# Performance work log

Hardware: AMD Instinct MI355X
Metric: run time of the kernel (lower is better)

The kernel has to match this reference:

```python
import jax, jax.numpy as jnp
import numpy as np

D = 1024
H = 16
HD = D // H


def setup_inputs() -> dict:
    key = jax.random.key(0)
    ks = jax.random.split(key, 5)
    s = 1.0 / np.sqrt(D)
    return {
        "inputs": jax.random.normal(ks[0], (2, 2048, D), dtype=jnp.float32),
        "Wq": jax.random.normal(ks[1], (D, D), dtype=jnp.float32) * s,
        "bq": jnp.zeros((D,), jnp.float32),
        "Wk": jax.random.normal(ks[2], (D, D), dtype=jnp.float32) * s,
        "bk": jnp.zeros((D,), jnp.float32),
        "Wv": jax.random.normal(ks[3], (D, D), dtype=jnp.float32) * s,
        "bv": jnp.zeros((D,), jnp.float32),
        "Wo": jax.random.normal(ks[4], (D, D), dtype=jnp.float32) * s,
        "bo": jnp.zeros((D,), jnp.float32),
    }


def reference(inputs, Wq, bq, Wk, bk, Wv, bv, Wo, bo):
    B, S, _ = inputs.shape
    def split_heads(x):  # [B,S,D] -> [B,H,S,hd]
        return x.reshape(B, S, H, HD).transpose(0, 2, 1, 3)
    q = split_heads(inputs @ Wq + bq)
    k = split_heads(inputs @ Wk + bk)
    v = split_heads(inputs @ Wv + bv)
    scale = 1.0 / jnp.sqrt(jnp.asarray(HD, inputs.dtype))
    scores = jnp.einsum("bhsd,bhtd->bhst", q, k) * scale  # [B,H,S,S]
    weights = jax.nn.softmax(scores, axis=-1)
    attn = jnp.einsum("bhst,bhtd->bhsd", weights, v)
    concat = attn.transpose(0, 2, 1, 3).reshape(B, S, D)
    return concat @ Wo + bo
```

## Files before the change

kernel.cpp:

```cpp
#include <hip/hip_runtime.h>


typedef __bf16 bf16x8 __attribute__((ext_vector_type(8)));
typedef float  f32x4  __attribute__((ext_vector_type(4)));

#if __has_builtin(__builtin_amdgcn_exp2f)
#define EXPFN(x) __builtin_amdgcn_exp2f(x)
#define QSCALE (0.125f * 1.44269504088896f)
#else
#define EXPFN(x) __expf(x)
#define QSCALE 0.125f
#endif

#define VMCNT(n)  asm volatile("s_waitcnt vmcnt(" #n ")" ::: "memory")
#define LGKMCNT0() asm volatile("s_waitcnt lgkmcnt(0)" ::: "memory")
#define BARRIER() __builtin_amdgcn_s_barrier()
#define WAIT0_BARRIER() asm volatile("s_waitcnt vmcnt(0)\n\ts_barrier" ::: "memory")

__device__ __forceinline__ unsigned short f2bf(float f) {
    unsigned int u = __float_as_uint(f);
    u += 0x7FFFu + ((u >> 16) & 1u);
    return (unsigned short)(u >> 16);
}

__device__ __forceinline__ void gload16(const void* g, void* l) {
    __builtin_amdgcn_global_load_lds(
        (const __attribute__((address_space(1))) void*)g,
        (__attribute__((address_space(3))) void*)l, 16, 0, 0);
}

__global__ __launch_bounds__(256) void prep_kernel(
    const float* __restrict__ X, ushort4* __restrict__ Xb,
    const float* __restrict__ Wq, const float* __restrict__ Wk,
    const float* __restrict__ Wv, const float* __restrict__ Wo,
    unsigned short* __restrict__ Wt_all) {
    const int z = blockIdx.z;
    if (z == 4) {
        int base = (blockIdx.y * 32 + blockIdx.x) * 1024 + threadIdx.x;
        const float4* X4 = (const float4*)X;
        #pragma unroll
        for (int c = 0; c < 4; c++) {
            int i = base + c * 256;
            float4 v = X4[i];
            ushort4 o;
            o.x = f2bf(v.x); o.y = f2bf(v.y); o.z = f2bf(v.z); o.w = f2bf(v.w);
            Xb[i] = o;
        }
        return;
    }
    __shared__ float tile[32][33];
    const float* W = (z == 0) ? Wq : (z == 1) ? Wk : (z == 2) ? Wv : Wo;
    unsigned short* Wt = Wt_all + (size_t)z * 1024 * 1024;
    int c0 = blockIdx.x * 32, r0 = blockIdx.y * 32;
    int x = threadIdx.x & 31, y = threadIdx.x >> 5;
    for (int j = 0; j < 32; j += 8)
        tile[y + j][x] = W[(r0 + y + j) * 1024 + c0 + x];
    __syncthreads();
    for (int j = 0; j < 32; j += 8)
        Wt[(c0 + y + j) * 1024 + r0 + x] = f2bf(tile[x][y + j]);
}

__global__ __launch_bounds__(256, 2) void gemm_qkv_kernel(
    const unsigned short* __restrict__ Xb, const unsigned short* __restrict__ Wt_all,
    const float* __restrict__ bq, const float* __restrict__ bk,
    const float* __restrict__ bv,
    unsigned short* __restrict__ Qb, unsigned short* __restrict__ Kb,
    unsigned short* __restrict__ Vt) {
    const int x0 = blockIdx.x * 128;
    const int y0 = blockIdx.y * 64;

    __shared__ __align__(16) unsigned short smem[128 * 64 + 3 * 64 * 64];
    unsigned short* As  = smem;
    unsigned short* Bqs = smem + 8192;
    unsigned short* Bks = smem + 12288;
    unsigned short* Bvs = smem + 16384;

    const unsigned short* Ap  = Xb + (size_t)x0 * 1024;
    const unsigned short* Bqp = Wt_all + (size_t)y0 * 1024;
    const unsigned short* Bkp = Wt_all + 1048576u + (size_t)y0 * 1024;
    const unsigned short* Bvp = Wt_all + 2097152u + (size_t)y0 * 1024;

    const int tid = threadIdx.x;
    const int lane = tid & 63, wave = tid >> 6;
    const int quad = lane >> 4, l15 = lane & 15;
    const int wrow = (wave >> 1) * 64, wcol = (wave & 1) * 32;

    f32x4 aq[4][2] = {};
    f32x4 ak[4][2] = {};
    f32x4 av[4][2] = {};

    const int srow = lane >> 3;
    const int ch8  = (lane & 7) * 8;
    const int swz  = (((lane & 7) ^ srow)) * 8;
    const int sw   = (l15 & 7);

    for (int k0 = 0; k0 < 1024; k0 += 64) {
        #pragma unroll
        for (int c = 0; c < 4; c++) {
            int r = c * 32 + wave * 8 + srow;
            gload16(Ap + (size_t)r * 1024 + k0 + swz, &As[r * 64 + ch8]);
        }
        #pragma unroll
        for (int c = 0; c < 2; c++) {
            int r = c * 32 + wave * 8 + srow;
            gload16(Bqp + (size_t)r * 1024 + k0 + swz, &Bqs[r * 64 + ch8]);
            gload16(Bkp + (size_t)r * 1024 + k0 + swz, &Bks[r * 64 + ch8]);
            gload16(Bvp + (size_t)r * 1024 + k0 + swz, &Bvs[r * 64 + ch8]);
        }
        WAIT0_BARRIER();
        #pragma unroll
        for (int kk = 0; kk < 2; kk++) {
            bf16x8 af[4], bqf[2], bkf[2], bvf[2];
            const int co = (((kk * 4 + quad) ^ sw)) * 8;
            #pragma unroll
            for (int i = 0; i < 4; i++)
                af[i] = *(const bf16x8*)&As[(wrow + i * 16 + l15) * 64 + co];
            #pragma unroll
            for (int j = 0; j < 2; j++) {
                bqf[j] = *(const bf16x8*)&Bqs[(wcol + j * 16 + l15) * 64 + co];
                bkf[j] = *(const bf16x8*)&Bks[(wcol + j * 16 + l15) * 64 + co];
                bvf[j] = *(const bf16x8*)&Bvs[(wcol + j * 16 + l15) * 64 + co];
            }
            #pragma unroll
            for (int i = 0; i < 4; i++)
                #pragma unroll
                for (int j = 0; j < 2; j++) {
                    aq[i][j] = __builtin_amdgcn_mfma_f32_16x16x32_bf16(
                        af[i], bqf[j], aq[i][j], 0, 0, 0);
                    ak[i][j] = __builtin_amdgcn_mfma_f32_16x16x32_bf16(
                        af[i], bkf[j], ak[i][j], 0, 0, 0);
                    av[i][j] = __builtin_amdgcn_mfma_f32_16x16x32_bf16(
                        af[i], bvf[j], av[i][j], 0, 0, 0);
                }
        }
        __syncthreads();
    }

    #pragma unroll
    for (int j = 0; j < 2; j++) {
        int col = y0 + wcol + j * 16 + l15;
        float bqc = bq[col], bkc = bk[col];
        int h = col >> 6, d = col & 63;
        #pragma unroll
        for (int i = 0; i < 4; i++)
            #pragma unroll
            for (int r = 0; r < 4; r++) {
                int row = x0 + wrow + i * 16 + quad * 4 + r;
                int b = row >> 11, s = row & 2047;
                size_t idx = (size_t)((b * 16 + h) * 2048 + s) * 64 + d;
                Qb[idx] = f2bf((aq[i][j][r] + bqc) * QSCALE);
                Kb[idx] = f2bf(ak[i][j][r] + bkc);
            }
    }

    __syncthreads();
    unsigned short* vts = smem;
    #pragma unroll
    for (int j = 0; j < 2; j++) {
        int n = wcol + j * 16 + l15;
        float bvc = bv[y0 + n];
        #pragma unroll
        for (int i = 0; i < 4; i++)
            #pragma unroll
            for (int r = 0; r < 4; r++) {
                int m = wrow + i * 16 + quad * 4 + r;
                vts[n * 136 + m] = f2bf(av[i][j][r] + bvc);
            }
    }
    __syncthreads();
    const int bseq = x0 >> 11;
    const int s0 = x0 & 2047;
    #pragma unroll
    for (int q = 0; q < 4; q++) {
        int c = q * 256 + tid;
        int n = c >> 4, mc = c & 15;
        uint4 vv = *(const uint4*)&vts[n * 136 + mc * 8];
        *(uint4*)&Vt[(size_t)(bseq * 1024 + y0 + n) * 2048 + s0 + mc * 8] = vv;
    }
}

__global__ __launch_bounds__(256) void attn_kernel(
    const unsigned short* __restrict__ Qb, const unsigned short* __restrict__ Kb,
    const unsigned short* __restrict__ Vt, unsigned short* __restrict__ Cc,
    float* __restrict__ Op, float* __restrict__ Lp, int tlen, int do_split) {
    const int bh = blockIdx.y;
    const int b = bh >> 4, h = bh & 15;
    const int q0 = blockIdx.x * 128;
    const int split = blockIdx.z;
    const int tbeg = split * tlen;

    const int tid = threadIdx.x;
    const int lane = tid & 63, wave = tid >> 6;
    const int quad = lane >> 4, l15 = lane & 15;

    __shared__ __align__(16) unsigned short Ks[2][64 * 64];
    __shared__ __align__(16) unsigned short Vs[2][64 * 64];

    const unsigned short* Qbh = Qb + (size_t)bh * 2048 * 64;
    const unsigned short* Kbh = Kb + (size_t)bh * 2048 * 64;
    const unsigned short* Vbh = Vt + (size_t)bh * 64 * 2048;

    bf16x8 qa[2][2];
    #pragma unroll
    for (int mi = 0; mi < 2; mi++)
        #pragma unroll
        for (int kk = 0; kk < 2; kk++)
            qa[mi][kk] = *(const bf16x8*)&Qbh[
                (size_t)(q0 + wave * 32 + mi * 16 + l15) * 64 + kk * 32 + quad * 8];

    union { unsigned short us[8]; bf16x8 v; } ones_u;
    #pragma unroll
    for (int i = 0; i < 8; i++) ones_u.us[i] = 0x3F80;
    const bf16x8 onesv = ones_u.v;

    f32x4 o[2][4] = {};
    f32x4 ol[2] = {};

    const int srow = lane >> 3;
    const int r0s = wave * 16 + srow;
    const int ch8 = (lane & 7) * 8;
    const int swz = (((lane & 7) ^ srow)) * 8;
    const int sw  = (l15 & 7);

    const int pk0 = (r0s & 0x23) | ((r0s & 0x0C) << 1) | ((r0s & 0x10) >> 2);
    const int r8  = r0s + 8;
    const int pk8 = (r8 & 0x23) | ((r8 & 0x0C) << 1) | ((r8 & 0x10) >> 2);

    auto stage = [&](int buf, int t0) {
        gload16(&Kbh[(size_t)(t0 + pk0) * 64 + swz],       &Ks[buf][r0s * 64 + ch8]);
        gload16(&Kbh[(size_t)(t0 + pk8) * 64 + swz],       &Ks[buf][(r0s + 8) * 64 + ch8]);
        gload16(&Vbh[(size_t)r0s * 2048 + t0 + swz],       &Vs[buf][r0s * 64 + ch8]);
        gload16(&Vbh[(size_t)(r0s + 8) * 2048 + t0 + swz], &Vs[buf][(r0s + 8) * 64 + ch8]);
    };

    stage(0, tbeg);
    int cur = 0;
    for (int ti = 0; ti < tlen; ti += 64) {
        if (ti + 64 < tlen) {
            stage(cur ^ 1, tbeg + ti + 64);
            VMCNT(4);
        } else {
            VMCNT(0);
        }
        BARRIER();
        const unsigned short* Ksc = Ks[cur];
        const unsigned short* Vsc = Vs[cur];

        f32x4 sf[2][4] = {};
        #pragma unroll
        for (int j = 0; j < 4; j++)
            #pragma unroll
            for (int kk = 0; kk < 2; kk++) {
                bf16x8 kf = *(const bf16x8*)&Ksc[(j * 16 + l15) * 64 +
                                                 (((kk * 4 + quad) ^ sw)) * 8];
                sf[0][j] = __builtin_amdgcn_mfma_f32_16x16x32_bf16(kf, qa[0][kk], sf[0][j], 0, 0, 0);
                sf[1][j] = __builtin_amdgcn_mfma_f32_16x16x32_bf16(kf, qa[1][kk], sf[1][j], 0, 0, 0);
            }

        union { unsigned int u[4]; bf16x8 v; } pa[2][2];
        #pragma unroll
        for (int mi = 0; mi < 2; mi++) {
            float pe[4][4];
            #pragma unroll
            for (int j = 0; j < 4; j++)
                #pragma unroll
                for (int r = 0; r < 4; r++)
                    pe[j][r] = EXPFN(sf[mi][j][r]);
            #pragma unroll
            for (int kk = 0; kk < 2; kk++)
                #pragma unroll
                for (int d = 0; d < 4; d++) {
                    const int j = 2 * kk + (d >> 1);
                    const int r = 2 * (d & 1);
                    unsigned int w;
                    asm("v_cvt_pk_bf16_f32 %0, %1, %2"
                        : "=v"(w) : "v"(pe[j][r]), "v"(pe[j][r + 1]));
                    pa[mi][kk].u[d] = w;
                }
        }

        #pragma unroll
        for (int kk = 0; kk < 2; kk++) {
            bf16x8 pf0 = pa[0][kk].v;
            bf16x8 pf1 = pa[1][kk].v;
            ol[0] = __builtin_amdgcn_mfma_f32_16x16x32_bf16(pf0, onesv, ol[0], 0, 0, 0);
            ol[1] = __builtin_amdgcn_mfma_f32_16x16x32_bf16(pf1, onesv, ol[1], 0, 0, 0);
            #pragma unroll
            for (int j = 0; j < 4; j++) {
                bf16x8 vf = *(const bf16x8*)&Vsc[(j * 16 + l15) * 64 +
                                                 (((kk * 4 + quad) ^ sw)) * 8];
                o[0][j] = __builtin_amdgcn_mfma_f32_16x16x32_bf16(pf0, vf, o[0][j], 0, 0, 0);
                o[1][j] = __builtin_amdgcn_mfma_f32_16x16x32_bf16(pf1, vf, o[1][j], 0, 0, 0);
            }
        }
        LGKMCNT0();
        BARRIER();
        cur ^= 1;
    }

    if (do_split) {
        float* Opd = Op + (size_t)(split * 32 + bh) * 2048 * 64;
        float* Lpd = Lp + (size_t)(split * 32 + bh) * 2048;
        #pragma unroll
        for (int mi = 0; mi < 2; mi++)
            #pragma unroll
            for (int r = 0; r < 4; r++) {
                int s = q0 + wave * 32 + mi * 16 + quad * 4 + r;
                if (l15 == 0) Lpd[s] = ol[mi][r];
                #pragma unroll
                for (int j = 0; j < 4; j++)
                    Opd[(size_t)s * 64 + j * 16 + l15] = o[mi][j][r];
            }
    } else {
        #pragma unroll
        for (int mi = 0; mi < 2; mi++)
            #pragma unroll
            for (int r = 0; r < 4; r++) {
                float inv = 1.f / ol[mi][r];
                int s = q0 + wave * 32 + mi * 16 + quad * 4 + r;
                size_t row = (size_t)(b * 2048 + s);
                #pragma unroll
                for (int j = 0; j < 4; j++)
                    Cc[row * 1024 + h * 64 + j * 16 + l15] = f2bf(o[mi][j][r] * inv);
            }
    }
}

__global__ __launch_bounds__(256) void combine_kernel(
    const float4* __restrict__ Op, const float* __restrict__ Lp,
    unsigned short* __restrict__ Cc) {
    int idx = blockIdx.x * 256 + threadIdx.x;
    int d4 = idx & 15;
    int s = (idx >> 4) & 2047;
    int bh = idx >> 15;
    const size_t half4 = (size_t)32 * 2048 * 16;
    float4 a = Op[(size_t)idx], c = Op[half4 + (size_t)idx];
    float l = Lp[bh * 2048 + s] + Lp[32 * 2048 + bh * 2048 + s];
    float inv = 1.f / l;
    ushort4 o;
    o.x = f2bf((a.x + c.x) * inv); o.y = f2bf((a.y + c.y) * inv);
    o.z = f2bf((a.z + c.z) * inv); o.w = f2bf((a.w + c.w) * inv);
    int b = bh >> 4, h = bh & 15;
    *(ushort4*)&Cc[((size_t)(b * 2048 + s)) * 1024 + h * 64 + d4 * 4] = o;
}

__global__ __launch_bounds__(256) void gemm_out_kernel(
    const unsigned short* __restrict__ Cc, const unsigned short* __restrict__ Wot,
    const float* __restrict__ bo, float* __restrict__ out) {
    const int m0 = blockIdx.x * 128;
    const int n0 = blockIdx.y * 64;

    __shared__ __align__(16) unsigned short As[128 * 64];
    __shared__ __align__(16) unsigned short Bs[64 * 64];

    const int tid = threadIdx.x;
    const int lane = tid & 63, wave = tid >> 6;
    const int quad = lane >> 4, l15 = lane & 15;
    const int wrow = (wave >> 1) * 64, wcol = (wave & 1) * 32;

    f32x4 acc[4][2] = {};
    const int srow = lane >> 3;
    const int ch8 = (lane & 7) * 8;
    const int swz = (((lane & 7) ^ srow)) * 8;
    const int sw  = (l15 & 7);

    for (int k0 = 0; k0 < 1024; k0 += 64) {
        #pragma unroll
        for (int c = 0; c < 4; c++) {
            int r = c * 32 + wave * 8 + srow;
            gload16(Cc + (size_t)(m0 + r) * 1024 + k0 + swz, &As[r * 64 + ch8]);
            if (c < 2)
                gload16(Wot + (size_t)(n0 + r) * 1024 + k0 + swz, &Bs[r * 64 + ch8]);
        }
        WAIT0_BARRIER();
        #pragma unroll
        for (int kk = 0; kk < 2; kk++) {
            bf16x8 af[4], bfr[2];
            #pragma unroll
            for (int i = 0; i < 4; i++)
                af[i] = *(const bf16x8*)&As[(wrow + i * 16 + l15) * 64 +
                                            (((kk * 4 + quad) ^ sw)) * 8];
            #pragma unroll
            for (int j = 0; j < 2; j++)
                bfr[j] = *(const bf16x8*)&Bs[(wcol + j * 16 + l15) * 64 +
                                             (((kk * 4 + quad) ^ sw)) * 8];
            #pragma unroll
            for (int i = 0; i < 4; i++)
                #pragma unroll
                for (int j = 0; j < 2; j++)
                    acc[i][j] = __builtin_amdgcn_mfma_f32_16x16x32_bf16(
                        af[i], bfr[j], acc[i][j], 0, 0, 0);
        }
        __syncthreads();
    }

    #pragma unroll
    for (int j = 0; j < 2; j++) {
        int col = n0 + wcol + j * 16 + l15;
        float bcol = bo[col];
        #pragma unroll
        for (int i = 0; i < 4; i++)
            #pragma unroll
            for (int r = 0; r < 4; r++) {
                int row = m0 + wrow + i * 16 + quad * 4 + r;
                out[(size_t)row * 1024 + col] = acc[i][j][r] + bcol;
            }
    }
}

extern "C" void kernel_launch(void* const* d_in, const int* in_sizes, int n_in,
                              void* d_out, int out_size, void* d_ws, size_t ws_size,
                              hipStream_t stream) {
    const float* X  = (const float*)d_in[0];
    const float* Wq = (const float*)d_in[1];
    const float* bq = (const float*)d_in[2];
    const float* Wk = (const float*)d_in[3];
    const float* bk = (const float*)d_in[4];
    const float* Wv = (const float*)d_in[5];
    const float* bv = (const float*)d_in[6];
    const float* Wo = (const float*)d_in[7];
    const float* bo = (const float*)d_in[8];
    float* out = (float*)d_out;

    char* ws = (char*)d_ws;
    unsigned short* Xb = (unsigned short*)(ws);
    unsigned short* Wt = (unsigned short*)(ws + (8u  << 20));
    unsigned short* Qb = (unsigned short*)(ws + (16u << 20));
    unsigned short* Kb = (unsigned short*)(ws + (24u << 20));
    unsigned short* Vt = (unsigned short*)(ws + (32u << 20));
    unsigned short* Cc = (unsigned short*)(ws + (40u << 20));
    float* Op = (float*)(ws + (48u << 20));
    float* Lp = (float*)(ws + (48u << 20) + 33554432u);
    const bool use_split = ws_size >= ((size_t)(48u << 20) + 33554432u + 524288u);

    prep_kernel<<<dim3(32, 32, 5), 256, 0, stream>>>(X, (ushort4*)Xb, Wq, Wk, Wv, Wo, Wt);
    gemm_qkv_kernel<<<dim3(32, 16), 256, 0, stream>>>(Xb, Wt, bq, bk, bv, Qb, Kb, Vt);
    if (use_split) {
        attn_kernel<<<dim3(16, 32, 2), 256, 0, stream>>>(Qb, Kb, Vt, Cc, Op, Lp, 1024, 1);
        combine_kernel<<<4096, 256, 0, stream>>>((const float4*)Op, Lp, Cc);
    } else {
        attn_kernel<<<dim3(16, 32, 1), 256, 0, stream>>>(Qb, Kb, Vt, Cc, Op, Lp, 2048, 0);
    }
    gemm_out_kernel<<<dim3(32, 16), 256, 0, stream>>>(Cc, Wt + 3u * 1024 * 1024, bo, out);
}
```

Baseline: 186.1 us.

## Remap block indices for XCD-aware L2 locality and add MFMA priority hints

Block IDs in the QKV GEMM, attention and output GEMM kernels are remapped so that blocks dispatched round-robin to the same XCD share weight columns or the same (batch, head) K/V data. The aim is better reuse in each XCD's private L2. The attention kernel also raises wave priority around its MFMA sections with s_setprio, so matrix work is favoured over the softmax exponent phase of other waves. The remap hardcodes the grid shapes (32x16 GEMM grids, 16x32xZ attention grid) and would silently break if the launch dimensions change.

Measured after the change: 191.5 us. 1.03x slower.

```diff
diff --git a/kernel.cpp b/kernel.cpp
--- a/kernel.cpp
+++ b/kernel.cpp
@@ -66,8 +66,12 @@
     const float* __restrict__ bv,
     unsigned short* __restrict__ Qb, unsigned short* __restrict__ Kb,
     unsigned short* __restrict__ Vt) {
-    const int x0 = blockIdx.x * 128;
-    const int y0 = blockIdx.y * 64;
+    const int n = blockIdx.x + 32 * blockIdx.y;
+    const int xcd = n & 7, s = n >> 3;
+    const int yb = xcd * 2 + (s >> 5);
+    const int xb = s & 31;
+    const int x0 = xb * 128;
+    const int y0 = yb * 64;
 
     __shared__ __align__(16) unsigned short smem[128 * 64 + 3 * 64 * 64];
     unsigned short* As  = smem;
@@ -146,8 +150,8 @@
             #pragma unroll
             for (int r = 0; r < 4; r++) {
                 int row = x0 + wrow + i * 16 + quad * 4 + r;
-                int b = row >> 11, s = row & 2047;
-                size_t idx = (size_t)((b * 16 + h) * 2048 + s) * 64 + d;
+                int b = row >> 11, s2 = row & 2047;
+                size_t idx = (size_t)((b * 16 + h) * 2048 + s2) * 64 + d;
                 Qb[idx] = f2bf((aq[i][j][r] + bqc) * QSCALE);
                 Kb[idx] = f2bf(ak[i][j][r] + bkc);
             }
@@ -157,14 +161,14 @@
     unsigned short* vts = smem;
     #pragma unroll
     for (int j = 0; j < 2; j++) {
-        int n = wcol + j * 16 + l15;
-        float bvc = bv[y0 + n];
+        int nn = wcol + j * 16 + l15;
+        float bvc = bv[y0 + nn];
         #pragma unroll
         for (int i = 0; i < 4; i++)
             #pragma unroll
             for (int r = 0; r < 4; r++) {
                 int m = wrow + i * 16 + quad * 4 + r;
-                vts[n * 136 + m] = f2bf(av[i][j][r] + bvc);
+                vts[nn * 136 + m] = f2bf(av[i][j][r] + bvc);
             }
     }
     __syncthreads();
@@ -173,9 +177,9 @@
     #pragma unroll
     for (int q = 0; q < 4; q++) {
         int c = q * 256 + tid;
-        int n = c >> 4, mc = c & 15;
-        uint4 vv = *(const uint4*)&vts[n * 136 + mc * 8];
-        *(uint4*)&Vt[(size_t)(bseq * 1024 + y0 + n) * 2048 + s0 + mc * 8] = vv;
+        int nn = c >> 4, mc = c & 15;
+        uint4 vv = *(const uint4*)&vts[nn * 136 + mc * 8];
+        *(uint4*)&Vt[(size_t)(bseq * 1024 + y0 + nn) * 2048 + s0 + mc * 8] = vv;
     }
 }
 
@@ -183,10 +187,16 @@
     const unsigned short* __restrict__ Qb, const unsigned short* __restrict__ Kb,
     const unsigned short* __restrict__ Vt, unsigned short* __restrict__ Cc,
     float* __restrict__ Op, float* __restrict__ Lp, int tlen, int do_split) {
-    const int bh = blockIdx.y;
+    const int zs = do_split ? 2 : 1;
+    const int n = blockIdx.x + 16 * (blockIdx.y + 32 * blockIdx.z);
+    const int xcd = n & 7, sl = n >> 3;
+    const int G = zs * 4;
+    const int g = xcd * G + (sl >> 4);
+    const int bh = g & 31;
+    const int split = g >> 5;
+    const int q0 = (sl & 15) * 128;
+
     const int b = bh >> 4, h = bh & 15;
-    const int q0 = blockIdx.x * 128;
-    const int split = blockIdx.z;
     const int tbeg = split * tlen;
 
     const int tid = threadIdx.x;
@@ -247,6 +257,7 @@
         const unsigned short* Vsc = Vs[cur];
 
         f32x4 sf[2][4] = {};
+        __builtin_amdgcn_s_setprio(1);
         #pragma unroll
         for (int j = 0; j < 4; j++)
             #pragma unroll
@@ -256,6 +267,7 @@
                 sf[0][j] = __builtin_amdgcn_mfma_f32_16x16x32_bf16(kf, qa[0][kk], sf[0][j], 0, 0, 0);
                 sf[1][j] = __builtin_amdgcn_mfma_f32_16x16x32_bf16(kf, qa[1][kk], sf[1][j], 0, 0, 0);
             }
+        __builtin_amdgcn_s_setprio(0);
 
         union { unsigned int u[4]; bf16x8 v; } pa[2][2];
         #pragma unroll
@@ -279,6 +291,7 @@
                 }
         }
 
+        __builtin_amdgcn_s_setprio(1);
         #pragma unroll
         for (int kk = 0; kk < 2; kk++) {
             bf16x8 pf0 = pa[0][kk].v;
@@ -293,6 +306,7 @@
                 o[1][j] = __builtin_amdgcn_mfma_f32_16x16x32_bf16(pf1, vf, o[1][j], 0, 0, 0);
             }
         }
+        __builtin_amdgcn_s_setprio(0);
         LGKMCNT0();
         BARRIER();
         cur ^= 1;
@@ -305,11 +319,11 @@
         for (int mi = 0; mi < 2; mi++)
             #pragma unroll
             for (int r = 0; r < 4; r++) {
-                int s = q0 + wave * 32 + mi * 16 + quad * 4 + r;
-                if (l15 == 0) Lpd[s] = ol[mi][r];
+                int s2 = q0 + wave * 32 + mi * 16 + quad * 4 + r;
+                if (l15 == 0) Lpd[s2] = ol[mi][r];
                 #pragma unroll
                 for (int j = 0; j < 4; j++)
-                    Opd[(size_t)s * 64 + j * 16 + l15] = o[mi][j][r];
+                    Opd[(size_t)s2 * 64 + j * 16 + l15] = o[mi][j][r];
             }
     } else {
         #pragma unroll
@@ -317,8 +331,8 @@
             #pragma unroll
             for (int r = 0; r < 4; r++) {
                 float inv = 1.f / ol[mi][r];
-                int s = q0 + wave * 32 + mi * 16 + quad * 4 + r;
-                size_t row = (size_t)(b * 2048 + s);
+                int s2 = q0 + wave * 32 + mi * 16 + quad * 4 + r;
+                size_t row = (size_t)(b * 2048 + s2);
                 #pragma unroll
                 for (int j = 0; j < 4; j++)
                     Cc[row * 1024 + h * 64 + j * 16 + l15] = f2bf(o[mi][j][r] * inv);
@@ -347,8 +361,12 @@
 __global__ __launch_bounds__(256) void gemm_out_kernel(
     const unsigned short* __restrict__ Cc, const unsigned short* __restrict__ Wot,
     const float* __restrict__ bo, float* __restrict__ out) {
-    const int m0 = blockIdx.x * 128;
-    const int n0 = blockIdx.y * 64;
+    const int n = blockIdx.x + 32 * blockIdx.y;
+    const int xcd = n & 7, s = n >> 3;
+    const int yb = xcd * 2 + (s >> 5);
+    const int xb = s & 31;
+    const int m0 = xb * 128;
+    const int n0 = yb * 64;
 
     __shared__ __align__(16) unsigned short As[128 * 64];
     __shared__ __align__(16) unsigned short Bs[64 * 64];
```
